# Optimization experiments

Hardware: AMD Instinct MI355X
Metric: run time of the kernel (lower is better)

## Reference

```python
import jax, jax.numpy as jnp
import numpy as np

V = 32000   # vocab_size
D = 64      # rnn_size == input_size (hard-coded in InstEncoder)
B = 16384   # batch
T = 64      # instruction length


def setup_inputs() -> dict:
    key = jax.random.key(0)
    ks = jax.random.split(key, 24)
    s = 0.05
    inp = {}
    # tokens in [1, V] so every position is non-zero -> last hidden is the final LSTM state
    inp['inst'] = jax.random.randint(ks[0], (B, T), 1, V + 1, dtype=jnp.int32)
    # canvas cells: [color, shape, row, col], small non-negative ints, stored as float
    inp['canvas'] = jax.random.randint(ks[1], (B, 25, 4), 0, 5).astype(jnp.float32)
    # 1 = absolute instruction, 2 = relative instruction
    inp['inst_type'] = jax.random.randint(ks[2], (B,), 1, 3, dtype=jnp.int32)
    # parameters
    inp['embed'] = jax.random.normal(ks[3], (V + 1, D)) * s
    inp['W_ih'] = jax.random.normal(ks[4], (D, 4 * D)) * s
    inp['W_hh'] = jax.random.normal(ks[5], (D, 4 * D)) * s
    inp['b_ih'] = jnp.zeros((4 * D,))
    inp['b_hh'] = jnp.zeros((4 * D,))
    inp['Wc'] = jax.random.normal(ks[6], (D, 3)) * s;  inp['bc'] = jnp.zeros((3,))
    inp['Ws'] = jax.random.normal(ks[7], (D, 3)) * s;  inp['bs'] = jnp.zeros((3,))
    inp['Wa'] = jax.random.normal(ks[8], (D, 2)) * s;  inp['ba'] = jnp.zeros((2,))
    inp['Wl'] = jax.random.normal(ks[9], (D, 25)) * s; inp['bl'] = jnp.zeros((25,))
    inp['Wr'] = jax.random.normal(ks[10], (D, 8)) * s; inp['br'] = jnp.zeros((8,))
    inp['Wr1'] = jax.random.normal(ks[11], (D + 4, 32)) * s; inp['br1'] = jnp.zeros((32,))
    inp['Wr2'] = jax.random.normal(ks[12], (32, 1)) * s;     inp['br2'] = jnp.zeros((1,))
    return inp


def _lstm_last_hidden(tokens, embed, W_ih, W_hh, b_ih, b_hh):
    x = embed[tokens]                      # [B, T, D]
    n = x.shape[0]
    h0 = jnp.zeros((n, D), x.dtype)
    c0 = jnp.zeros((n, D), x.dtype)

    def step(carry, xt):
        h, c = carry
        gates = xt @ W_ih + h @ W_hh + (b_ih + b_hh)   # [B, 4D], torch gate order i,f,g,o
        i, f, g, o = jnp.split(gates, 4, axis=-1)
        c = jax.nn.sigmoid(f) * c + jax.nn.sigmoid(i) * jnp.tanh(g)
        h = jax.nn.sigmoid(o) * jnp.tanh(c)
        return (h, c), None

    (h, _), _ = jax.lax.scan(step, (h0, c0), jnp.swapaxes(x, 0, 1))
    return h                               # [B, D]


def _sample_head(logits, k):
    logp = jax.nn.log_softmax(logits, axis=-1)
    samp = jax.random.categorical(k, logits, axis=-1)
    lp = jnp.take_along_axis(logp, samp[:, None], axis=-1)[:, 0]
    return samp, lp


def reference(inst, canvas, inst_type, embed, W_ih, W_hh, b_ih, b_hh,
              Wc, bc, Ws, bs, Wa, ba, Wl, bl, Wr, br, Wr1, br1, Wr2, br2):
    n = inst.shape[0]
    e = _lstm_last_hidden(inst, embed, W_ih, W_hh, b_ih, b_hh)   # [B, 64]

    key = jax.random.key(42)
    k_color, k_shape, k_act, k_abs, k_rel, k_att = jax.random.split(key, 6)

    color_s, color_lp = _sample_head(e @ Wc + bc, k_color)   # 3-way
    shape_s, shape_lp = _sample_head(e @ Ws + bs, k_shape)   # 3-way
    act_s,   act_lp   = _sample_head(e @ Wa + ba, k_act)     # 2-way (pred_act=True)

    # absolute location head: 25-way
    abs_loc_s, abs_loc_lp = _sample_head(e @ Wl + bl, k_abs)

    # relative: 8-way offset head + ref-object attention over 25 canvas cells
    rel_s, rel_lp = _sample_head(e @ Wr + br, k_rel)
    att_in = jnp.concatenate(
        [jnp.broadcast_to(e[:, None, :], (n, 25, D)), canvas], axis=-1)   # [B, 25, 68]
    att_logits = (jax.nn.relu(att_in @ Wr1 + br1) @ Wr2 + br2)[..., 0]    # [B, 25]
    att_s, att_lp = _sample_head(att_logits, k_att)
    # gather the attended canvas cell (vectorized version of the per-row .cpu() loop)
    ref_obj = jnp.take_along_axis(canvas, att_s[:, None, None], axis=1)[:, 0, :].astype(jnp.int32)

    offsets = jnp.array([[-1, 0], [1, 0], [0, 1], [0, -1],
                         [-1, -1], [-1, 1], [1, -1], [1, 1]], dtype=jnp.int32)
    off = offsets[rel_s]                                                  # [B, 2]
    rel_loc = (ref_obj[:, 2] + off[:, 0]) * 5 + (ref_obj[:, 3] + off[:, 1])

    # vectorized index_join: ref_type 0 -> abs path, 1 -> rel path
    is_rel = (inst_type - 1) == 1
    loc_predict = jnp.where(is_rel, rel_loc, abs_loc_s.astype(jnp.int32))
    loc_lp = jnp.where(is_rel, rel_lp, abs_loc_lp)
    att_lp = jnp.where(is_rel, att_lp, jnp.zeros_like(att_lp))

    log_probs = jnp.stack([color_lp, shape_lp, act_lp, loc_lp, att_lp], axis=-1)  # [B, 5]
    return log_probs, loc_predict
```

## Files before the change

kernel.cpp:

```cpp
#include <hip/hip_runtime.h>
#include <hip/hip_bf16.h>
#include <stdint.h>


__device__ __forceinline__ uint32_t rotl32(uint32_t x, uint32_t r) {
  return (x << r) | (x >> (32u - r));
}

__device__ __forceinline__ uint2 threefry2x32(uint32_t k0, uint32_t k1,
                                              uint32_t x0, uint32_t x1) {
  const uint32_t k2 = k0 ^ k1 ^ 0x1BD11BDAu;
  x0 += k0; x1 += k1;
#define TFR(r) { x0 += x1; x1 = rotl32(x1, r); x1 ^= x0; }
  TFR(13u) TFR(15u) TFR(26u) TFR(6u)
  x0 += k1; x1 += k2 + 1u;
  TFR(17u) TFR(29u) TFR(16u) TFR(24u)
  x0 += k2; x1 += k0 + 2u;
  TFR(13u) TFR(15u) TFR(26u) TFR(6u)
  x0 += k0; x1 += k1 + 3u;
  TFR(17u) TFR(29u) TFR(16u) TFR(24u)
  x0 += k1; x1 += k2 + 4u;
  TFR(13u) TFR(15u) TFR(26u) TFR(6u)
  x0 += k2; x1 += k0 + 5u;
#undef TFR
  return make_uint2(x0, x1);
}

__device__ __forceinline__ float gumbel_jax(uint32_t k0, uint32_t k1, uint32_t idx) {
  uint2 o = threefry2x32(k0, k1, 0u, idx);
  uint32_t bits = o.x ^ o.y;
  float f = __uint_as_float(0x3f800000u | (bits >> 9)) - 1.0f;
  const float tiny = 1.1754943508222875e-38f;
  float u = fmaxf(tiny, f + tiny);
  return -logf(-logf(u));
}

template <int C>
__device__ __forceinline__ void sample_head(const float* lg, uint32_t k0, uint32_t k1,
                                            int row, int& samp, float& lp) {
  float best = -3.402823466e38f;
  int bi = 0;
  float lsel = lg[0];
  float m = lg[0];
  #pragma unroll
  for (int c = 0; c < C; ++c) {
    float t = lg[c] + gumbel_jax(k0, k1, (uint32_t)(row * C + c));
    if (t > best) { best = t; bi = c; lsel = lg[c]; }
    m = fmaxf(m, lg[c]);
  }
  float s = 0.f;
  #pragma unroll
  for (int c = 0; c < C; ++c) s += expf(lg[c] - m);
  samp = bi;
  lp = lsel - m - logf(s);
}

__device__ __forceinline__ float sigmoidf_(float x) { return 1.0f / (1.0f + expf(-x)); }

__global__ __launch_bounds__(1024) void k_embedw(
    const float* __restrict__ embed, const float* __restrict__ W_ih,
    const float* __restrict__ b_ih, const float* __restrict__ b_hh,
    float* __restrict__ embedWG, int NV) {
  __shared__ float sW[64 * 256];
  const int tid = threadIdx.x;
  for (int i = tid; i < 4096; i += 1024)
    ((float4*)sW)[i] = ((const float4*)W_ih)[i];
  __syncthreads();
  const int d   = tid & 63;
  const int gi  = (tid >> 6) & 3;
  const int vr0 = tid >> 8;
  const int g   = gi * 64 + d;
  const float bias = b_ih[g] + b_hh[g];
  const int vbase = blockIdx.x * 126;
  for (int it = 0; it < 32; ++it) {
    int lr = it * 4 + vr0;
    int v  = vbase + lr;
    if (lr < 126 && v < NV) {
      const float* e = embed + (size_t)v * 64;
      float acc = bias;
      #pragma unroll 8
      for (int k = 0; k < 64; ++k) acc = fmaf(e[k], sW[k * 256 + g], acc);
      embedWG[(size_t)v * 256 + d * 4 + gi] = acc;
    }
  }
}

__global__ __launch_bounds__(1024) void k_wt(const float* __restrict__ W_hh,
                                             float* __restrict__ wt) {
  const int idx = blockIdx.x * 1024 + threadIdx.x;
  if (idx < 16384) {
    const int k = idx >> 8, g = idx & 255;
    const int gi = g >> 6, u = g & 63;
    wt[k * 256 + u * 4 + gi] = W_hh[idx];
  }
}

__global__ __launch_bounds__(1024) void k_lstm64(
    const int* __restrict__ inst, const float* __restrict__ wt,
    const float* __restrict__ embedWG, float* __restrict__ eOut) {
  __shared__ float sH[4096];

  const int tid = threadIdx.x;
  const int l   = tid & 63;
  const int wid = tid >> 6;
  const int d0  = wid << 2;
  const int rbase = blockIdx.x << 6;
  const size_t r  = (size_t)rbase + l;

  const float* __restrict__ wp = wt + __builtin_amdgcn_readfirstlane(wid * 16);

  for (int i = tid; i < 4096; i += 1024) sH[i] = 0.f;
  __syncthreads();

  float c[4] = {0.f, 0.f, 0.f, 0.f};
  float4 gc[4], gn[4];
  int tok1;
  {
    int tok0 = inst[r * 64 + 0];
    tok1     = inst[r * 64 + 1];
    const float4* p = (const float4*)(embedWG + (size_t)tok0 * 256 + d0 * 4);
    #pragma unroll
    for (int i = 0; i < 4; ++i) gc[i] = p[i];
  }

  for (int t = 0; t < 64; ++t) {
    {
      const float4* p = (const float4*)(embedWG + (size_t)tok1 * 256 + d0 * 4);
      #pragma unroll
      for (int i = 0; i < 4; ++i) gn[i] = p[i];
    }
    int tok2 = inst[r * 64 + (t + 2 < 64 ? t + 2 : 63)];

    float a[4][4];
    #pragma unroll
    for (int u = 0; u < 4; ++u) {
      a[u][0] = gc[u].x; a[u][1] = gc[u].y; a[u][2] = gc[u].z; a[u][3] = gc[u].w;
    }

    #pragma unroll 4
    for (int k = 0; k < 64; ++k) {
      float hk = sH[k * 64 + l];
      const float* __restrict__ wk = wp + k * 256;
      #pragma unroll
      for (int j = 0; j < 16; ++j)
        a[j >> 2][j & 3] = fmaf(hk, wk[j], a[j >> 2][j & 3]);
    }
    __syncthreads();
    #pragma unroll
    for (int u = 0; u < 4; ++u) {
      float ig = sigmoidf_(a[u][0]);
      float fg = sigmoidf_(a[u][1]);
      float gg = tanhf(a[u][2]);
      float og = sigmoidf_(a[u][3]);
      float cn = fg * c[u] + ig * gg;
      c[u] = cn;
      sH[(d0 + u) * 64 + l] = og * tanhf(cn);
    }
    __syncthreads();
    #pragma unroll
    for (int i = 0; i < 4; ++i) gc[i] = gn[i];
    tok1 = tok2;
  }

  for (int i = tid; i < 4096; i += 1024) {
    int rr = i >> 6, dd = i & 63;
    eOut[(size_t)(rbase + rr) * 64 + dd] = sH[dd * 64 + rr];
  }
}

__global__ __launch_bounds__(256) void k_attlog(
    const float* __restrict__ eOut, const float* __restrict__ canvas,
    const float* __restrict__ Wr1, const float* __restrict__ br1,
    const float* __restrict__ Wr2, const float* __restrict__ br2,
    float* __restrict__ attL, int total) {
  const int gid = blockIdx.x * 256 + threadIdx.x;
  if (gid >= total) return;
  const int rrow = gid / 25, cell = gid - rrow * 25;
  const float* e  = eOut + (size_t)rrow * 64;
  const float* cv = canvas + (size_t)rrow * 100 + cell * 4;
  float cv0 = cv[0], cv1 = cv[1], cv2 = cv[2], cv3 = cv[3];

  float h[32];
  #pragma unroll
  for (int j4 = 0; j4 < 8; ++j4) {
    float4 b4 = ((const float4*)br1)[j4];
    float4 w64 = ((const float4*)(Wr1 + 64 * 32))[j4];
    float4 w65 = ((const float4*)(Wr1 + 65 * 32))[j4];
    float4 w66 = ((const float4*)(Wr1 + 66 * 32))[j4];
    float4 w67 = ((const float4*)(Wr1 + 67 * 32))[j4];
    h[j4*4+0] = fmaf(cv3, w67.x, fmaf(cv2, w66.x, fmaf(cv1, w65.x, fmaf(cv0, w64.x, b4.x))));
    h[j4*4+1] = fmaf(cv3, w67.y, fmaf(cv2, w66.y, fmaf(cv1, w65.y, fmaf(cv0, w64.y, b4.y))));
    h[j4*4+2] = fmaf(cv3, w67.z, fmaf(cv2, w66.z, fmaf(cv1, w65.z, fmaf(cv0, w64.z, b4.z))));
    h[j4*4+3] = fmaf(cv3, w67.w, fmaf(cv2, w66.w, fmaf(cv1, w65.w, fmaf(cv0, w64.w, b4.w))));
  }
  for (int k = 0; k < 64; ++k) {
    float ek = e[k];
    const float4* wrow = (const float4*)(Wr1 + k * 32);
    #pragma unroll
    for (int j4 = 0; j4 < 8; ++j4) {
      float4 w = wrow[j4];
      h[j4*4+0] = fmaf(ek, w.x, h[j4*4+0]);
      h[j4*4+1] = fmaf(ek, w.y, h[j4*4+1]);
      h[j4*4+2] = fmaf(ek, w.z, h[j4*4+2]);
      h[j4*4+3] = fmaf(ek, w.w, h[j4*4+3]);
    }
  }
  float logit = br2[0];
  #pragma unroll
  for (int j = 0; j < 32; ++j) logit = fmaf(fmaxf(h[j], 0.f), Wr2[j], logit);
  attL[gid] = logit;
}

__global__ __launch_bounds__(256) void k_heads(
    const float* __restrict__ eOut, const float* __restrict__ canvas,
    const int* __restrict__ inst_type,
    const float* __restrict__ Wc, const float* __restrict__ bc,
    const float* __restrict__ Wsh, const float* __restrict__ bsh,
    const float* __restrict__ Wa, const float* __restrict__ ba,
    const float* __restrict__ Wl, const float* __restrict__ bl,
    const float* __restrict__ Wr, const float* __restrict__ br,
    const float* __restrict__ attL, float* __restrict__ out, int B) {
  const int r = blockIdx.x * 256 + threadIdx.x;
  if (r >= B) return;
  const float* e = eOut + (size_t)r * 64;

  uint2 kc  = threefry2x32(0u, 42u, 0u, 0u);
  uint2 ksh = threefry2x32(0u, 42u, 0u, 1u);
  uint2 kac = threefry2x32(0u, 42u, 0u, 2u);
  uint2 kab = threefry2x32(0u, 42u, 0u, 3u);
  uint2 krl = threefry2x32(0u, 42u, 0u, 4u);
  uint2 kat = threefry2x32(0u, 42u, 0u, 5u);

  float lc[3]  = {bc[0], bc[1], bc[2]};
  float lsh[3] = {bsh[0], bsh[1], bsh[2]};
  float lac[2] = {ba[0], ba[1]};
  float ll[25];
  #pragma unroll
  for (int j = 0; j < 25; ++j) ll[j] = bl[j];
  float lrr[8];
  #pragma unroll
  for (int j = 0; j < 8; ++j) lrr[j] = br[j];

  for (int k = 0; k < 64; ++k) {
    float ek = e[k];
    #pragma unroll
    for (int j = 0; j < 3; ++j)  lc[j]  = fmaf(ek, Wc[k * 3 + j],  lc[j]);
    #pragma unroll
    for (int j = 0; j < 3; ++j)  lsh[j] = fmaf(ek, Wsh[k * 3 + j], lsh[j]);
    #pragma unroll
    for (int j = 0; j < 2; ++j)  lac[j] = fmaf(ek, Wa[k * 2 + j],  lac[j]);
    #pragma unroll
    for (int j = 0; j < 25; ++j) ll[j]  = fmaf(ek, Wl[k * 25 + j], ll[j]);
    #pragma unroll
    for (int j = 0; j < 8; ++j)  lrr[j] = fmaf(ek, Wr[k * 8 + j],  lrr[j]);
  }

  int s_color, s_shape, s_act, s_abs, s_rel, s_att;
  float lp_color, lp_shape, lp_act, lp_abs, lp_rel, lp_att;
  sample_head<3>(lc,  kc.x,  kc.y,  r, s_color, lp_color);
  sample_head<3>(lsh, ksh.x, ksh.y, r, s_shape, lp_shape);
  sample_head<2>(lac, kac.x, kac.y, r, s_act,   lp_act);
  sample_head<25>(ll, kab.x, kab.y, r, s_abs,   lp_abs);
  sample_head<8>(lrr, krl.x, krl.y, r, s_rel,   lp_rel);

  float lat[25];
  #pragma unroll
  for (int j = 0; j < 25; ++j) lat[j] = attL[(size_t)r * 25 + j];
  sample_head<25>(lat, kat.x, kat.y, r, s_att, lp_att);

  const float* cvp = canvas + (size_t)r * 100 + s_att * 4;
  int ref_r = (int)cvp[2];
  int ref_c = (int)cvp[3];
  int dr = (int)((0x22001120u >> (4 * s_rel)) & 15u) - 1;
  int dc = (int)((0x20200211u >> (4 * s_rel)) & 15u) - 1;
  int rel_loc = (ref_r + dr) * 5 + (ref_c + dc);

  bool isrel = (inst_type[r] == 2);
  out[(size_t)r * 5 + 0] = lp_color;
  out[(size_t)r * 5 + 1] = lp_shape;
  out[(size_t)r * 5 + 2] = lp_act;
  out[(size_t)r * 5 + 3] = isrel ? lp_rel : lp_abs;
  out[(size_t)r * 5 + 4] = isrel ? lp_att : 0.f;
  out[(size_t)B * 5 + r] = (float)(isrel ? rel_loc : s_abs);
}

extern "C" void kernel_launch(void* const* d_in, const int* in_sizes, int n_in,
                              void* d_out, int out_size, void* d_ws, size_t ws_size,
                              hipStream_t stream) {
  (void)n_in; (void)out_size; (void)ws_size;
  const int*   inst      = (const int*)  d_in[0];
  const float* canvas    = (const float*)d_in[1];
  const int*   inst_type = (const int*)  d_in[2];
  const float* embed     = (const float*)d_in[3];
  const float* W_ih      = (const float*)d_in[4];
  const float* W_hh      = (const float*)d_in[5];
  const float* b_ih      = (const float*)d_in[6];
  const float* b_hh      = (const float*)d_in[7];
  const float* Wc  = (const float*)d_in[8];  const float* bc  = (const float*)d_in[9];
  const float* Wsh = (const float*)d_in[10]; const float* bsh = (const float*)d_in[11];
  const float* Wa  = (const float*)d_in[12]; const float* ba  = (const float*)d_in[13];
  const float* Wl  = (const float*)d_in[14]; const float* bl  = (const float*)d_in[15];
  const float* Wr  = (const float*)d_in[16]; const float* br  = (const float*)d_in[17];
  const float* Wr1 = (const float*)d_in[18]; const float* br1 = (const float*)d_in[19];
  const float* Wr2 = (const float*)d_in[20]; const float* br2 = (const float*)d_in[21];

  const int B  = in_sizes[0] / 64;
  const int NV = in_sizes[3] / 64;

  float* embedWG = (float*)d_ws;
  float* eOut    = embedWG + (size_t)NV * 256;
  float* attL    = eOut + (size_t)B * 64;
  float* wtbuf   = attL + (size_t)B * 25;
  float* out     = (float*)d_out;

  k_embedw<<<(NV + 125) / 126, 1024, 0, stream>>>(embed, W_ih, b_ih, b_hh, embedWG, NV);
  k_wt<<<16, 1024, 0, stream>>>(W_hh, wtbuf);
  k_lstm64<<<B / 64, 1024, 0, stream>>>(inst, wtbuf, embedWG, eOut);
  {
    int total = B * 25;
    k_attlog<<<(total + 255) / 256, 256, 0, stream>>>(eOut, canvas, Wr1, br1, Wr2, br2,
                                                      attL, total);
  }
  k_heads<<<(B + 255) / 256, 256, 0, stream>>>(eOut, canvas, inst_type,
                                               Wc, bc, Wsh, bsh, Wa, ba, Wl, bl, Wr, br,
                                               attL, out, B);
}
```

Baseline: 841.5 us.

## Double-buffer LSTM hidden state and use packed FMA with prefetched weights

The LSTM recurrence kernel now keeps the hidden state in two shared-memory buffers, which removes one of the two barriers per timestep. The inner 64x16 FMA loop uses v_pk_fma_f32 inline asm on float pairs, with wave-uniform weights in scalar registers, and prefetches the next k's weights. This is meant to halve the vector FMA instruction count and reduce barrier stalls. In exchange the kernel uses twice the LDS and more scalar registers, and the final readout relies on the last step writing buffer 0.

```diff
diff --git a/kernel.cpp b/kernel.cpp
--- a/kernel.cpp
+++ b/kernel.cpp
@@ -2,6 +2,11 @@
 #include <hip/hip_bf16.h>
 #include <stdint.h>
 
+
+typedef float v2f __attribute__((ext_vector_type(2)));
+struct W16 { v2f p[8]; };
+
+#define PKFMA(A, W, H) asm("v_pk_fma_f32 %0, %1, %2, %0" : "+v"(A) : "s"(W), "v"(H))
 
 __device__ __forceinline__ uint32_t rotl32(uint32_t x, uint32_t r) {
   return (x << r) | (x >> (32u - r));
@@ -98,7 +103,7 @@
 __global__ __launch_bounds__(1024) void k_lstm64(
     const int* __restrict__ inst, const float* __restrict__ wt,
     const float* __restrict__ embedWG, float* __restrict__ eOut) {
-  __shared__ float sH[4096];
+  __shared__ float sH[2][4096];
 
   const int tid = threadIdx.x;
   const int l   = tid & 63;
@@ -109,62 +114,73 @@
 
   const float* __restrict__ wp = wt + __builtin_amdgcn_readfirstlane(wid * 16);
 
-  for (int i = tid; i < 4096; i += 1024) sH[i] = 0.f;
+  for (int i = tid; i < 4096; i += 1024) sH[0][i] = 0.f;
   __syncthreads();
 
   float c[4] = {0.f, 0.f, 0.f, 0.f};
-  float4 gc[4], gn[4];
+  v2f gc[8], gn[8];
   int tok1;
   {
     int tok0 = inst[r * 64 + 0];
     tok1     = inst[r * 64 + 1];
-    const float4* p = (const float4*)(embedWG + (size_t)tok0 * 256 + d0 * 4);
-    #pragma unroll
-    for (int i = 0; i < 4; ++i) gc[i] = p[i];
-  }
-
+    const v2f* p = (const v2f*)(embedWG + (size_t)tok0 * 256 + d0 * 4);
+    #pragma unroll
+    for (int i = 0; i < 8; ++i) gc[i] = p[i];
+  }
+
+  int cur = 0;
   for (int t = 0; t < 64; ++t) {
     {
-      const float4* p = (const float4*)(embedWG + (size_t)tok1 * 256 + d0 * 4);
+      const v2f* p = (const v2f*)(embedWG + (size_t)tok1 * 256 + d0 * 4);
       #pragma unroll
-      for (int i = 0; i < 4; ++i) gn[i] = p[i];
+      for (int i = 0; i < 8; ++i) gn[i] = p[i];
     }
     int tok2 = inst[r * 64 + (t + 2 < 64 ? t + 2 : 63)];
 
-    float a[4][4];
-    #pragma unroll
-    for (int u = 0; u < 4; ++u) {
-      a[u][0] = gc[u].x; a[u][1] = gc[u].y; a[u][2] = gc[u].z; a[u][3] = gc[u].w;
-    }
-
+    const float* sHc = sH[cur];
+    float*       sHn = sH[cur ^ 1];
+
+    v2f acc[8];
+    #pragma unroll
+    for (int j = 0; j < 8; ++j) acc[j] = gc[j];
+
+    W16 wcur = *(const W16*)(wp + 0);
     #pragma unroll 4
     for (int k = 0; k < 64; ++k) {
-      float hk = sH[k * 64 + l];
-      const float* __restrict__ wk = wp + k * 256;
-      #pragma unroll
-      for (int j = 0; j < 16; ++j)
-        a[j >> 2][j & 3] = fmaf(hk, wk[j], a[j >> 2][j & 3]);
-    }
-    __syncthreads();
+      W16 wnxt = *(const W16*)(wp + ((k + 1) & 63) * 256);
+      float hk = sHc[k * 64 + l];
+      v2f h2; h2[0] = hk; h2[1] = hk;
+      PKFMA(acc[0], wcur.p[0], h2);
+      PKFMA(acc[1], wcur.p[1], h2);
+      PKFMA(acc[2], wcur.p[2], h2);
+      PKFMA(acc[3], wcur.p[3], h2);
+      PKFMA(acc[4], wcur.p[4], h2);
+      PKFMA(acc[5], wcur.p[5], h2);
+      PKFMA(acc[6], wcur.p[6], h2);
+      PKFMA(acc[7], wcur.p[7], h2);
+      wcur = wnxt;
+    }
+
     #pragma unroll
     for (int u = 0; u < 4; ++u) {
-      float ig = sigmoidf_(a[u][0]);
-      float fg = sigmoidf_(a[u][1]);
-      float gg = tanhf(a[u][2]);
-      float og = sigmoidf_(a[u][3]);
+      float ig = sigmoidf_(acc[2 * u][0]);
+      float fg = sigmoidf_(acc[2 * u][1]);
+      float gg = tanhf(acc[2 * u + 1][0]);
+      float og = sigmoidf_(acc[2 * u + 1][1]);
       float cn = fg * c[u] + ig * gg;
       c[u] = cn;
-      sH[(d0 + u) * 64 + l] = og * tanhf(cn);
+      sHn[(d0 + u) * 64 + l] = og * tanhf(cn);
     }
     __syncthreads();
-    #pragma unroll
-    for (int i = 0; i < 4; ++i) gc[i] = gn[i];
+    cur ^= 1;
+    #pragma unroll
+    for (int i = 0; i < 8; ++i) gc[i] = gn[i];
     tok1 = tok2;
   }
 
   for (int i = tid; i < 4096; i += 1024) {
     int rr = i >> 6, dd = i & 63;
-    eOut[(size_t)(rbase + rr) * 64 + dd] = sH[dd * 64 + rr];
+    eOut[(size_t)(rbase + rr) * 64 + dd] = sH[0][dd * 64 + rr];
   }
 }
 
```

Measured after the change: 860.2 us. 2.2% more time.

## Restructure LSTM kernel into 16-row blocks with double-buffered hidden state

Applied to the files above, without the earlier changes.

The LSTM recurrence kernel now processes 16 batch rows per 256-thread block instead of 64 rows per 1024-thread block. Each lane owns one row and four hidden units, and the recurrent weights are read as float4 with the next step's weights prefetched. The hidden state is double-buffered in shared memory, so only one barrier per timestep is needed instead of two. This raises block count and cuts synchronization. The trade-off is that weight reads are no longer wave-uniform scalar loads but per-lane vector loads, which may add cache traffic.

```diff
diff --git a/kernel.cpp b/kernel.cpp
--- a/kernel.cpp
+++ b/kernel.cpp
@@ -95,76 +95,99 @@
   }
 }
 
-__global__ __launch_bounds__(1024) void k_lstm64(
+__global__ __launch_bounds__(256) void k_lstm64(
     const int* __restrict__ inst, const float* __restrict__ wt,
     const float* __restrict__ embedWG, float* __restrict__ eOut) {
-  __shared__ float sH[4096];
+  __shared__ float hs[2][1024];
 
   const int tid = threadIdx.x;
+  const int w   = tid >> 6;
   const int l   = tid & 63;
-  const int wid = tid >> 6;
-  const int d0  = wid << 2;
-  const int rbase = blockIdx.x << 6;
-  const size_t r  = (size_t)rbase + l;
-
-  const float* __restrict__ wp = wt + __builtin_amdgcn_readfirstlane(wid * 16);
-
-  for (int i = tid; i < 4096; i += 1024) sH[i] = 0.f;
-  __syncthreads();
-
-  float c[4] = {0.f, 0.f, 0.f, 0.f};
-  float4 gc[4], gn[4];
+  const int rr  = l & 15;
+  const int uu  = l >> 4;
+  const int ub  = w * 16 + uu * 4;
+  const int rbase = blockIdx.x << 4;
+  const int rowg  = rbase + rr;
+
+  for (int i = tid; i < 1024; i += 256) hs[0][i] = 0.f;
+
+  const float4* __restrict__ wt4 = (const float4*)wt;
+  const float4* __restrict__ eg4 = (const float4*)embedWG;
+
+  float c0 = 0.f, c1 = 0.f, c2 = 0.f, c3 = 0.f;
+  float4 gn0, gn1, gn2, gn3;
   int tok1;
   {
-    int tok0 = inst[r * 64 + 0];
-    tok1     = inst[r * 64 + 1];
-    const float4* p = (const float4*)(embedWG + (size_t)tok0 * 256 + d0 * 4);
-    #pragma unroll
-    for (int i = 0; i < 4; ++i) gc[i] = p[i];
-  }
-
+    int tok0 = inst[(size_t)rowg * 64 + 0];
+    tok1     = inst[(size_t)rowg * 64 + 1];
+    const float4* p = eg4 + (size_t)tok0 * 64 + ub;
+    gn0 = p[0]; gn1 = p[1]; gn2 = p[2]; gn3 = p[3];
+  }
+
+  float4 wc0 = wt4[ub], wc1 = wt4[ub + 1], wc2 = wt4[ub + 2], wc3 = wt4[ub + 3];
+
+  __syncthreads();
+
+  int cur = 0;
   for (int t = 0; t < 64; ++t) {
-    {
-      const float4* p = (const float4*)(embedWG + (size_t)tok1 * 256 + d0 * 4);
-      #pragma unroll
-      for (int i = 0; i < 4; ++i) gn[i] = p[i];
-    }
-    int tok2 = inst[r * 64 + (t + 2 < 64 ? t + 2 : 63)];
-
-    float a[4][4];
-    #pragma unroll
-    for (int u = 0; u < 4; ++u) {
-      a[u][0] = gc[u].x; a[u][1] = gc[u].y; a[u][2] = gc[u].z; a[u][3] = gc[u].w;
-    }
-
-    #pragma unroll 4
+    const float* hc = hs[cur];
+    float*       hn = hs[cur ^ 1];
+
+    float4 A0 = gn0, A1 = gn1, A2 = gn2, A3 = gn3;
+
+    {
+      const float4* p = eg4 + (size_t)tok1 * 64 + ub;
+      gn0 = p[0]; gn1 = p[1]; gn2 = p[2]; gn3 = p[3];
+    }
+    int tok2 = inst[(size_t)rowg * 64 + ((t + 2) & 63)];
+
     for (int k = 0; k < 64; ++k) {
-      float hk = sH[k * 64 + l];
-      const float* __restrict__ wk = wp + k * 256;
-      #pragma unroll
-      for (int j = 0; j < 16; ++j)
-        a[j >> 2][j & 3] = fmaf(hk, wk[j], a[j >> 2][j & 3]);
+      float hk = hc[k * 16 + rr];
+      const float4* wp = wt4 + ((k + 1) & 63) * 64 + ub;
+      float4 n0 = wp[0], n1 = wp[1], n2 = wp[2], n3 = wp[3];
+      A0.x = fmaf(hk, wc0.x, A0.x); A0.y = fmaf(hk, wc0.y, A0.y);
+      A0.z = fmaf(hk, wc0.z, A0.z); A0.w = fmaf(hk, wc0.w, A0.w);
+      A1.x = fmaf(hk, wc1.x, A1.x); A1.y = fmaf(hk, wc1.y, A1.y);
+      A1.z = fmaf(hk, wc1.z, A1.z); A1.w = fmaf(hk, wc1.w, A1.w);
+      A2.x = fmaf(hk, wc2.x, A2.x); A2.y = fmaf(hk, wc2.y, A2.y);
+      A2.z = fmaf(hk, wc2.z, A2.z); A2.w = fmaf(hk, wc2.w, A2.w);
+      A3.x = fmaf(hk, wc3.x, A3.x); A3.y = fmaf(hk, wc3.y, A3.y);
+      A3.z = fmaf(hk, wc3.z, A3.z); A3.w = fmaf(hk, wc3.w, A3.w);
+      wc0 = n0; wc1 = n1; wc2 = n2; wc3 = n3;
+    }
+
+    {
+      float ig = sigmoidf_(A0.x), fg = sigmoidf_(A0.y);
+      float gg = tanhf(A0.z),     og = sigmoidf_(A0.w);
+      float cn = fg * c0 + ig * gg; c0 = cn;
+      hn[(ub + 0) * 16 + rr] = og * tanhf(cn);
+    }
+    {
+      float ig = sigmoidf_(A1.x), fg = sigmoidf_(A1.y);
+      float gg = tanhf(A1.z),     og = sigmoidf_(A1.w);
+      float cn = fg * c1 + ig * gg; c1 = cn;
+      hn[(ub + 1) * 16 + rr] = og * tanhf(cn);
+    }
+    {
+      float ig = sigmoidf_(A2.x), fg = sigmoidf_(A2.y);
+      float gg = tanhf(A2.z),     og = sigmoidf_(A2.w);
+      float cn = fg * c2 + ig * gg; c2 = cn;
+      hn[(ub + 2) * 16 + rr] = og * tanhf(cn);
+    }
+    {
+      float ig = sigmoidf_(A3.x), fg = sigmoidf_(A3.y);
+      float gg = tanhf(A3.z),     og = sigmoidf_(A3.w);
+      float cn = fg * c3 + ig * gg; c3 = cn;
+      hn[(ub + 3) * 16 + rr] = og * tanhf(cn);
     }
     __syncthreads();
-    #pragma unroll
-    for (int u = 0; u < 4; ++u) {
-      float ig = sigmoidf_(a[u][0]);
-      float fg = sigmoidf_(a[u][1]);
-      float gg = tanhf(a[u][2]);
-      float og = sigmoidf_(a[u][3]);
-      float cn = fg * c[u] + ig * gg;
-      c[u] = cn;
-      sH[(d0 + u) * 64 + l] = og * tanhf(cn);
-    }
-    __syncthreads();
-    #pragma unroll
-    for (int i = 0; i < 4; ++i) gc[i] = gn[i];
+    cur ^= 1;
     tok1 = tok2;
   }
 
-  for (int i = tid; i < 4096; i += 1024) {
-    int rr = i >> 6, dd = i & 63;
-    eOut[(size_t)(rbase + rr) * 64 + dd] = sH[dd * 64 + rr];
+  for (int i = tid; i < 1024; i += 256) {
+    int u = i & 63, r2 = i >> 6;
+    eOut[(size_t)(rbase + r2) * 64 + u] = hs[0][u * 16 + r2];
   }
 }
 
@@ -315,7 +338,7 @@
 
   k_embedw<<<(NV + 125) / 126, 1024, 0, stream>>>(embed, W_ih, b_ih, b_hh, embedWG, NV);
   k_wt<<<16, 1024, 0, stream>>>(W_hh, wtbuf);
-  k_lstm64<<<B / 64, 1024, 0, stream>>>(inst, wtbuf, embedWG, eOut);
+  k_lstm64<<<B / 16, 256, 0, stream>>>(inst, wtbuf, embedWG, eOut);
   {
     int total = B * 25;
     k_attlog<<<(total + 255) / 256, 256, 0, stream>>>(eOut, canvas, Wr1, br1, Wr2, br2,
```

Result: slower. 2.314 ms (+175.0%).
